# Kernel tuning notes

Measured on AMD Instinct MI355X. Metric: run time of the kernel, lower is better.

Reference implementation:

```python
import jax, jax.numpy as jnp
import numpy as np

N, E, F, U, H = 10000, 160000, 128, 128, 8
BN_EPS = 1e-3  # keras BatchNormalization default


def _batch_norm(x, gamma, beta):
    # GraphBatchNormalization in training mode: stats over the flat node/edge axis
    mean = jnp.mean(x, axis=0, keepdims=True)
    var = jnp.var(x, axis=0, keepdims=True)
    return (x - mean) * jax.lax.rsqrt(var + BN_EPS) * gamma + beta


def setup_inputs() -> dict:
    key = jax.random.key(0)
    k = jax.random.split(key, 12)
    s = 0.1  # weight init scale
    return {
        "node_attributes": jax.random.normal(k[0], (N, F), jnp.float32),
        "edge_attributes": jax.random.normal(k[1], (E, F), jnp.float32),
        "edge_indices": jax.random.randint(k[2], (E, 2), 0, N, jnp.int32),
        "W_edge": jax.random.normal(k[3], (3 * F, U), jnp.float32) * s,
        "b_edge": jnp.zeros((U,), jnp.float32),
        "gamma_e": jnp.ones((U,), jnp.float32),
        "beta_e": jnp.zeros((U,), jnp.float32),
        "W_node": jax.random.normal(k[4], (F, U), jnp.float32) * s,
        "b_node": jnp.zeros((U,), jnp.float32),
        "gamma_n": jnp.ones((U,), jnp.float32),
        "beta_n": jnp.zeros((U,), jnp.float32),
        "W_att": jax.random.normal(k[5], (H, F, U), jnp.float32) * s,
        "b_att": jnp.zeros((H, U), jnp.float32),
        "a_att": jax.random.normal(k[6], (H, 3 * U), jnp.float32) * s,
        "gru_kernel": jax.random.normal(k[7], (U, 3 * U), jnp.float32) * s,
        "gru_rkernel": jax.random.normal(k[8], (U, 3 * U), jnp.float32) * s,
        "gru_bias": jnp.zeros((2, 3 * U), jnp.float32),
    }


def reference(node_attributes, edge_attributes, edge_indices, W_edge, b_edge,
              gamma_e, beta_e, W_node, b_node, gamma_n, beta_n,
              W_att, b_att, a_att, gru_kernel, gru_rkernel, gru_bias):
    dst = edge_indices[:, 0]  # receiving (ingoing) node per edge
    src = edge_indices[:, 1]  # sending (outgoing) node per edge

    # gather -> concat -> edge MLP -> graph batch norm
    edge_in = node_attributes[src]   # GatherNodesOutgoing
    edge_out = node_attributes[dst]  # GatherNodesIngoing
    edge_concat = jnp.concatenate([edge_in, edge_out, edge_attributes], axis=-1)  # [E, 3F]
    edge_updated = jax.nn.relu(edge_concat @ W_edge + b_edge)
    edge_updated = _batch_norm(edge_updated, gamma_e, beta_e)  # [E, U]

    # multi-head GAT attention over edges, aggregated to receiving node
    z = jnp.einsum('nf,hfu->hnu', node_attributes, W_att) + b_att[:, None, :]  # [H,N,U]
    a_src, a_dst, a_edge = jnp.split(a_att, 3, axis=-1)  # each [H,U]
    s_src = jnp.einsum('hnu,hu->hn', z, a_src)[:, src]           # [H,E]
    s_dst = jnp.einsum('hnu,hu->hn', z, a_dst)[:, dst]           # [H,E]
    s_edge = jnp.einsum('eu,hu->he', edge_updated, a_edge)       # [H,E]
    logits = jax.nn.leaky_relu(s_src + s_dst + s_edge, 0.2)

    seg_max = jax.vmap(lambda l: jax.ops.segment_max(l, dst, num_segments=N))(logits)  # [H,N]
    ex = jnp.exp(logits - seg_max[:, dst])
    den = jax.vmap(lambda e: jax.ops.segment_sum(e, dst, num_segments=N))(ex)          # [H,N]
    alpha = ex / den[:, dst]                                                            # [H,E]

    msgs = alpha[:, :, None] * z[:, src]  # [H,E,U]
    agg = jax.vmap(lambda m: jax.ops.segment_sum(m, dst, num_segments=N))(msgs)  # [H,N,U]
    node_attended = jax.nn.relu(jnp.mean(agg, axis=0))  # [N,U]

    # node MLP + graph batch norm
    node_updated = jax.nn.relu(node_attributes @ W_node + b_node)
    node_updated = _batch_norm(node_updated, gamma_n, beta_n)  # [N,U]

    # GRU update (keras GRUCell, reset_after=True): input=node_attended, state=node_updated
    mx = node_attended @ gru_kernel + gru_bias[0]
    mi = node_updated @ gru_rkernel + gru_bias[1]
    xz, xr, xh = jnp.split(mx, 3, axis=-1)
    rz, rr, rh = jnp.split(mi, 3, axis=-1)
    zg = jax.nn.sigmoid(xz + rz)
    rg = jax.nn.sigmoid(xr + rr)
    hh = jnp.tanh(xh + rg * rh)
    node_final = zg * node_updated + (1.0 - zg) * hh

    return node_final, edge_updated
```

## Files before the change

kernel.cpp:

```cpp
#include <hip/hip_runtime.h>
#include <hip/hip_bf16.h>

#define NN 10000
#define EE 160000
#define FF 128
#define UU 128
#define HH 8
#define BN_EPS 1e-3f

typedef __attribute__((ext_vector_type(8))) short bf16x8;
typedef __attribute__((ext_vector_type(8))) unsigned short u16x8;
typedef __attribute__((ext_vector_type(4))) float f32x4;

static __device__ __forceinline__ unsigned short f2bf(float f) {
    unsigned u = __float_as_uint(f);
    u += 0x7fffu + ((u >> 16) & 1u);
    return (unsigned short)(u >> 16);
}
static __device__ __forceinline__ float bf2f(unsigned short b) {
    return __uint_as_float((unsigned)b << 16);
}

__global__ void k_prep(const float* __restrict__ node, unsigned short* __restrict__ node_bf,
                       const float* __restrict__ We, unsigned short* __restrict__ WtE,
                       const float* __restrict__ Wn, unsigned short* __restrict__ WnT,
                       const float* __restrict__ Watt, unsigned short* __restrict__ WtA,
                       const float* __restrict__ Wk, const float* __restrict__ Wr,
                       unsigned short* __restrict__ WcT) {
    int b = blockIdx.x, t = threadIdx.x;
    if (b < 1250) {
        int i = b * 256 + t;
        float4 v = reinterpret_cast<const float4*>(node)[i];
        ushort4 o;
        o.x = f2bf(v.x); o.y = f2bf(v.y); o.z = f2bf(v.z); o.w = f2bf(v.w);
        reinterpret_cast<ushort4*>(node_bf)[i] = o;
    } else if (b < 1442) {
        int i = (b - 1250) * 256 + t;
        int s = i >> 14, rem = i & 16383, u = rem >> 7, k = rem & 127;
        WtE[i] = f2bf(We[(s * 128 + k) * 128 + u]);
    } else if (b < 1506) {
        int i = (b - 1442) * 256 + t;
        int k = i >> 7, u = i & 127;
        WnT[u * 128 + k] = f2bf(Wn[i]);
    } else if (b < 2018) {
        int i = (b - 1506) * 256 + t;
        int h = i >> 14, rem = i & 16383, f = rem >> 7, u = rem & 127;
        WtA[h * 16384 + u * 128 + f] = f2bf(Watt[i]);
    } else {
        int i = (b - 2018) * 256 + t;
        int c = i >> 8, k = i & 255;
        float v;
        if (c < 256)       v = (k < 128) ? Wk[k * 384 + c] : Wr[(k - 128) * 384 + c];
        else if (c < 384)  v = (k < 128) ? Wk[k * 384 + c] : 0.f;
        else               v = (k < 128) ? 0.f : Wr[(k - 128) * 384 + (c - 128)];
        WcT[c * 256 + k] = f2bf(v);
    }
}

__global__ void k_hist(const int* __restrict__ eidx, int* __restrict__ cnt, int E) {
    int e = blockIdx.x * 256 + threadIdx.x;
    if (e < E) atomicAdd(&cnt[eidx[2 * e]], 1);
}

__global__ void k_scan(const int* __restrict__ cnt, int* __restrict__ off,
                       int* __restrict__ cursor, int N) {
    __shared__ int wpre[16];
    __shared__ int runsh;
    int t = threadIdx.x, lane = t & 63, wv = t >> 6;
    if (t == 0) { off[0] = 0; runsh = 0; }
    __syncthreads();
    for (int base = 0; base < N; base += 1024) {
        int x = (base + t < N) ? cnt[base + t] : 0;
        int s = x;
#pragma unroll
        for (int o = 1; o < 64; o <<= 1) {
            int v = __shfl_up(s, o, 64);
            if (lane >= o) s += v;
        }
        if (lane == 63) wpre[wv] = s;
        __syncthreads();
        if (t == 0) {
            int acc = runsh;
#pragma unroll
            for (int i = 0; i < 16; ++i) { int tmp = wpre[i]; wpre[i] = acc; acc += tmp; }
            runsh = acc;
        }
        __syncthreads();
        int inc = s + wpre[wv];
        if (base + t < N) {
            off[base + t + 1] = inc;
            cursor[base + t] = inc - x;
        }
        __syncthreads();
    }
}

__global__ void k_scatter(const int* __restrict__ eidx, int* __restrict__ cursor,
                          int* __restrict__ elist, int E) {
    int e = blockIdx.x * 256 + threadIdx.x;
    if (e < E) {
        int d = eidx[2 * e];
        int p = atomicAdd(&cursor[d], 1);
        elist[p] = e;
    }
}

__global__ void __launch_bounds__(256) k_z8(
        const unsigned short* __restrict__ node_bf, const unsigned short* __restrict__ WtA,
        const float* __restrict__ batt, const float* __restrict__ aatt,
        unsigned short* __restrict__ zt, float* __restrict__ s_src, float* __restrict__ s_dst) {
    __shared__ unsigned short lds[16 * 1032];
    int n0 = blockIdx.x * 16;
    int t = threadIdx.x;
    {
        int r = t >> 4, c = t & 15;
        *reinterpret_cast<uint4*>(&lds[r * 136 + c * 8]) =
            *reinterpret_cast<const uint4*>(node_bf + (size_t)(n0 + r) * 128 + c * 8);
    }
    __syncthreads();

    int wid = t >> 6, lane = t & 63;
    int lr = lane & 15, lg = lane >> 4;

    f32x4 acc[2][8];
#pragma unroll
    for (int hh = 0; hh < 2; ++hh)
#pragma unroll
        for (int nt = 0; nt < 8; ++nt) acc[hh][nt] = (f32x4){0.f, 0.f, 0.f, 0.f};

#pragma unroll
    for (int ks = 0; ks < 4; ++ks) {
        int kb = ks * 32 + lg * 8;
        bf16x8 a = *reinterpret_cast<const bf16x8*>(&lds[lr * 136 + kb]);
#pragma unroll
        for (int hh = 0; hh < 2; ++hh) {
            const unsigned short* Wh = WtA + (size_t)(wid * 2 + hh) * 16384;
#pragma unroll
            for (int nt = 0; nt < 8; ++nt) {
                bf16x8 b = *reinterpret_cast<const bf16x8*>(Wh + (size_t)(nt * 16 + lr) * 128 + kb);
                acc[hh][nt] = __builtin_amdgcn_mfma_f32_16x16x32_bf16(a, b, acc[hh][nt], 0, 0, 0);
            }
        }
    }

    __syncthreads();
    float ps[2][4], pd[2][4];
#pragma unroll
    for (int hh = 0; hh < 2; ++hh)
#pragma unroll
        for (int r = 0; r < 4; ++r) { ps[hh][r] = 0.f; pd[hh][r] = 0.f; }

#pragma unroll
    for (int hh = 0; hh < 2; ++hh) {
        int head = wid * 2 + hh;
#pragma unroll
        for (int nt = 0; nt < 8; ++nt) {
            int col = nt * 16 + lr;
            float bias = batt[head * 128 + col];
            float as = aatt[head * 384 + col];
            float ad = aatt[head * 384 + 128 + col];
#pragma unroll
            for (int r = 0; r < 4; ++r) {
                int row = lg * 4 + r;
                float zval = acc[hh][nt][r] + bias;
                lds[row * 1032 + ((col * 8) ^ ((row & 3) << 4)) + head] = f2bf(zval);
                ps[hh][r] = fmaf(zval, as, ps[hh][r]);
                pd[hh][r] = fmaf(zval, ad, pd[hh][r]);
            }
        }
    }
#pragma unroll
    for (int o = 1; o < 16; o <<= 1) {
#pragma unroll
        for (int hh = 0; hh < 2; ++hh)
#pragma unroll
            for (int r = 0; r < 4; ++r) {
                ps[hh][r] += __shfl_xor(ps[hh][r], o, 64);
                pd[hh][r] += __shfl_xor(pd[hh][r], o, 64);
            }
    }
    if (lr == 0) {
#pragma unroll
        for (int hh = 0; hh < 2; ++hh) {
            int head = wid * 2 + hh;
#pragma unroll
            for (int r = 0; r < 4; ++r) {
                int n = n0 + lg * 4 + r;
                s_src[n * 8 + head] = ps[hh][r];
                s_dst[n * 8 + head] = pd[hh][r];
            }
        }
    }
    __syncthreads();
    for (int q = t; q < 16 * 128; q += 256) {
        int row = q >> 7, c = q & 127;
        *reinterpret_cast<uint4*>(&zt[(size_t)(n0 + row) * 1024 + c * 8]) =
            *reinterpret_cast<const uint4*>(&lds[row * 1032 + ((c * 8) ^ ((row & 3) << 4))]);
    }
}

__global__ void __launch_bounds__(256) k_p12_mfma(
        const unsigned short* __restrict__ node_bf, const unsigned short* __restrict__ WtE,
        unsigned short* __restrict__ p12, int N) {
    __shared__ unsigned short ash[64][136];
    int n0 = blockIdx.x * 64;
    int s = blockIdx.y;
    int t = threadIdx.x;
    for (int q = t; q < 64 * 16; q += 256) {
        int r = q >> 4, c = q & 15;
        int n = n0 + r; if (n >= N) n = N - 1;
        *reinterpret_cast<uint4*>(&ash[r][c * 8]) =
            *reinterpret_cast<const uint4*>(node_bf + (size_t)n * 128 + c * 8);
    }
    __syncthreads();

    int wid = t >> 6, lane = t & 63;
    int wm = wid >> 1, wn = wid & 1;
    int lr = lane & 15, lg = lane >> 4;

    f32x4 acc[2][4];
#pragma unroll
    for (int m = 0; m < 2; ++m)
#pragma unroll
        for (int n = 0; n < 4; ++n) acc[m][n] = (f32x4){0.f, 0.f, 0.f, 0.f};

    const unsigned short* Wh = WtE + (size_t)s * 16384;
#pragma unroll
    for (int ks = 0; ks < 4; ++ks) {
        int kb = ks * 32 + lg * 8;
        bf16x8 a0 = *reinterpret_cast<const bf16x8*>(&ash[wm * 32 + lr][kb]);
        bf16x8 a1 = *reinterpret_cast<const bf16x8*>(&ash[wm * 32 + 16 + lr][kb]);
        bf16x8 b[4];
#pragma unroll
        for (int n = 0; n < 4; ++n)
            b[n] = *reinterpret_cast<const bf16x8*>(Wh + (size_t)(wn * 64 + n * 16 + lr) * 128 + kb);
#pragma unroll
        for (int n = 0; n < 4; ++n) {
            acc[0][n] = __builtin_amdgcn_mfma_f32_16x16x32_bf16(a0, b[n], acc[0][n], 0, 0, 0);
            acc[1][n] = __builtin_amdgcn_mfma_f32_16x16x32_bf16(a1, b[n], acc[1][n], 0, 0, 0);
        }
    }

    __syncthreads();
    unsigned short* ot = &ash[0][0];
#pragma unroll
    for (int n = 0; n < 4; ++n) {
        int col = wn * 64 + n * 16 + lr;
#pragma unroll
        for (int m = 0; m < 2; ++m) {
            int rowb = wm * 32 + m * 16 + lg * 4;
#pragma unroll
            for (int r = 0; r < 4; ++r)
                ot[(rowb + r) * 136 + col] = f2bf(acc[m][n][r]);
        }
    }
    __syncthreads();
    for (int q = t; q < 64 * 16; q += 256) {
        int r = q >> 4, c = q & 15;
        int row = n0 + r;
        if (row < N)
            *reinterpret_cast<uint4*>(&p12[(size_t)row * 256 + s * 128 + c * 8]) =
                *reinterpret_cast<const uint4*>(&ot[r * 136 + c * 8]);
    }
}

__global__ void __launch_bounds__(256) k_pe_comb(
        const float* __restrict__ eattr, const unsigned short* __restrict__ WtE,
        const float* __restrict__ be, const unsigned short* __restrict__ p12,
        const int* __restrict__ eidx, unsigned short* __restrict__ ebuf,
        float* __restrict__ part) {
    __shared__ unsigned short ash[64][136];
    __shared__ int sd[128];
    __shared__ float sbuf[4][64], qbuf[4][64];
    int e0 = blockIdx.x * 64;
    int t = threadIdx.x;
    if (t < 128) sd[t] = eidx[e0 * 2 + t];
    for (int q = t; q < 64 * 32; q += 256) {
        int r = q >> 5, c = q & 31;
        float4 v = *reinterpret_cast<const float4*>(eattr + (size_t)(e0 + r) * 128 + c * 4);
        ushort4 o;
        o.x = f2bf(v.x); o.y = f2bf(v.y); o.z = f2bf(v.z); o.w = f2bf(v.w);
        *reinterpret_cast<ushort4*>(&ash[r][c * 4]) = o;
    }
    __syncthreads();

    int wid = t >> 6, lane = t & 63;
    int wm = wid >> 1, wn = wid & 1;
    int lr = lane & 15, lg = lane >> 4;

    f32x4 acc[2][4];
#pragma unroll
    for (int m = 0; m < 2; ++m)
#pragma unroll
        for (int n = 0; n < 4; ++n) acc[m][n] = (f32x4){0.f, 0.f, 0.f, 0.f};

    const unsigned short* Wh = WtE + (size_t)2 * 16384;
#pragma unroll
    for (int ks = 0; ks < 4; ++ks) {
        int kb = ks * 32 + lg * 8;
        bf16x8 a0 = *reinterpret_cast<const bf16x8*>(&ash[wm * 32 + lr][kb]);
        bf16x8 a1 = *reinterpret_cast<const bf16x8*>(&ash[wm * 32 + 16 + lr][kb]);
        bf16x8 b[4];
#pragma unroll
        for (int n = 0; n < 4; ++n)
            b[n] = *reinterpret_cast<const bf16x8*>(Wh + (size_t)(wn * 64 + n * 16 + lr) * 128 + kb);
#pragma unroll
        for (int n = 0; n < 4; ++n) {
            acc[0][n] = __builtin_amdgcn_mfma_f32_16x16x32_bf16(a0, b[n], acc[0][n], 0, 0, 0);
            acc[1][n] = __builtin_amdgcn_mfma_f32_16x16x32_bf16(a1, b[n], acc[1][n], 0, 0, 0);
        }
    }

    __syncthreads();
    for (int q = t; q < 64 * 16; q += 256) {
        int r = q >> 4, c = q & 15;
        int dst = sd[r * 2], src = sd[r * 2 + 1];
        u16x8 a = *reinterpret_cast<const u16x8*>(p12 + (size_t)src * 256 + c * 8);
        u16x8 b = *reinterpret_cast<const u16x8*>(p12 + (size_t)dst * 256 + 128 + c * 8);
        u16x8 o;
#pragma unroll
        for (int j = 0; j < 8; ++j) o[j] = f2bf(bf2f(a[j]) + bf2f(b[j]));
        *reinterpret_cast<u16x8*>(&ash[r][c * 8]) = o;
    }
    __syncthreads();

    unsigned short* ot = &ash[0][0];
    float s[4] = {0.f, 0.f, 0.f, 0.f}, q[4] = {0.f, 0.f, 0.f, 0.f};
#pragma unroll
    for (int n = 0; n < 4; ++n) {
        int col = wn * 64 + n * 16 + lr;
        float bias = be[col];
#pragma unroll
        for (int m = 0; m < 2; ++m) {
            int rowb = wm * 32 + m * 16 + lg * 4;
#pragma unroll
            for (int r = 0; r < 4; ++r) {
                int row = rowb + r;
                float v = acc[m][n][r] + bias + bf2f(ot[row * 136 + col]);
                v = v > 0.f ? v : 0.f;
                ot[row * 136 + col] = f2bf(v);
                s[n] += v;
                q[n] += v * v;
            }
        }
    }
#pragma unroll
    for (int n = 0; n < 4; ++n) {
        s[n] += __shfl_xor(s[n], 16, 64);
        s[n] += __shfl_xor(s[n], 32, 64);
        q[n] += __shfl_xor(q[n], 16, 64);
        q[n] += __shfl_xor(q[n], 32, 64);
    }
    if (lane < 16) {
#pragma unroll
        for (int n = 0; n < 4; ++n) {
            sbuf[wid][n * 16 + lane] = s[n];
            qbuf[wid][n * 16 + lane] = q[n];
        }
    }
    __syncthreads();
    for (int q2 = t; q2 < 64 * 16; q2 += 256) {
        int r = q2 >> 4, c = q2 & 15;
        *reinterpret_cast<uint4*>(&ebuf[(size_t)(e0 + r) * 128 + c * 8]) =
            *reinterpret_cast<const uint4*>(&ot[r * 136 + c * 8]);
    }
    if (t < 128) {
        int half = t >> 6, c = t & 63;
        part[(size_t)blockIdx.x * 256 + t] = sbuf[half][c] + sbuf[2 + half][c];
        part[(size_t)blockIdx.x * 256 + 128 + t] = qbuf[half][c] + qbuf[2 + half][c];
    }
}

__global__ void __launch_bounds__(256) k_node_mlp_mfma(
        const unsigned short* __restrict__ node_bf, const unsigned short* __restrict__ WnT,
        const float* __restrict__ bn, unsigned short* __restrict__ nupd_bf,
        float* __restrict__ part, int N) {
    __shared__ unsigned short ash[64][136];
    __shared__ float sbuf[4][64], qbuf[4][64];
    int n0 = blockIdx.x * 64;
    int t = threadIdx.x;
    for (int q = t; q < 64 * 16; q += 256) {
        int r = q >> 4, c = q & 15;
        int n = n0 + r; if (n >= N) n = N - 1;
        *reinterpret_cast<uint4*>(&ash[r][c * 8]) =
            *reinterpret_cast<const uint4*>(node_bf + (size_t)n * 128 + c * 8);
    }
    __syncthreads();

    int wid = t >> 6, lane = t & 63;
    int wm = wid >> 1, wn = wid & 1;
    int lr = lane & 15, lg = lane >> 4;

    f32x4 acc[2][4];
#pragma unroll
    for (int m = 0; m < 2; ++m)
#pragma unroll
        for (int n = 0; n < 4; ++n) acc[m][n] = (f32x4){0.f, 0.f, 0.f, 0.f};

#pragma unroll
    for (int ks = 0; ks < 4; ++ks) {
        int kb = ks * 32 + lg * 8;
        bf16x8 a0 = *reinterpret_cast<const bf16x8*>(&ash[wm * 32 + lr][kb]);
        bf16x8 a1 = *reinterpret_cast<const bf16x8*>(&ash[wm * 32 + 16 + lr][kb]);
        bf16x8 b[4];
#pragma unroll
        for (int n = 0; n < 4; ++n)
            b[n] = *reinterpret_cast<const bf16x8*>(WnT + (size_t)(wn * 64 + n * 16 + lr) * 128 + kb);
#pragma unroll
        for (int n = 0; n < 4; ++n) {
            acc[0][n] = __builtin_amdgcn_mfma_f32_16x16x32_bf16(a0, b[n], acc[0][n], 0, 0, 0);
            acc[1][n] = __builtin_amdgcn_mfma_f32_16x16x32_bf16(a1, b[n], acc[1][n], 0, 0, 0);
        }
    }

    __syncthreads();
    unsigned short* ot = &ash[0][0];
    float s[4] = {0.f, 0.f, 0.f, 0.f}, q[4] = {0.f, 0.f, 0.f, 0.f};
#pragma unroll
    for (int n = 0; n < 4; ++n) {
        int col = wn * 64 + n * 16 + lr;
        float bias = bn[col];
#pragma unroll
        for (int m = 0; m < 2; ++m) {
            int rowb = wm * 32 + m * 16 + lg * 4;
#pragma unroll
            for (int r = 0; r < 4; ++r) {
                int row = n0 + rowb + r;
                float v = acc[m][n][r] + bias;
                v = v > 0.f ? v : 0.f;
                ot[(rowb + r) * 136 + col] = f2bf(v);
                if (row < N) { s[n] += v; q[n] += v * v; }
            }
        }
    }
#pragma unroll
    for (int n = 0; n < 4; ++n) {
        s[n] += __shfl_xor(s[n], 16, 64);
        s[n] += __shfl_xor(s[n], 32, 64);
        q[n] += __shfl_xor(q[n], 16, 64);
        q[n] += __shfl_xor(q[n], 32, 64);
    }
    if (lane < 16) {
#pragma unroll
        for (int n = 0; n < 4; ++n) {
            sbuf[wid][n * 16 + lane] = s[n];
            qbuf[wid][n * 16 + lane] = q[n];
        }
    }
    __syncthreads();
    for (int q2 = t; q2 < 64 * 16; q2 += 256) {
        int r = q2 >> 4, c = q2 & 15;
        int row = n0 + r;
        if (row < N)
            *reinterpret_cast<uint4*>(&nupd_bf[(size_t)row * 128 + c * 8]) =
                *reinterpret_cast<const uint4*>(&ot[r * 136 + c * 8]);
    }
    if (t < 128) {
        int half = t >> 6, c = t & 63;
        part[(size_t)blockIdx.x * 256 + t] = sbuf[half][c] + sbuf[2 + half][c];
        part[(size_t)blockIdx.x * 256 + 128 + t] = qbuf[half][c] + qbuf[2 + half][c];
    }
}

__global__ void k_bn_fin(const float* __restrict__ part, int nblk, float invcnt,
                         const float* __restrict__ g, const float* __restrict__ b,
                         float* __restrict__ scale, float* __restrict__ shift) {
    int u = blockIdx.x;
    int t = threadIdx.x;
    float s = 0.f, q = 0.f;
    for (int i = t; i < nblk; i += 256) {
        s += part[(size_t)i * 256 + u];
        q += part[(size_t)i * 256 + 128 + u];
    }
    __shared__ float ls[4], lq[4];
    for (int o = 32; o > 0; o >>= 1) {
        s += __shfl_down(s, o, 64);
        q += __shfl_down(q, o, 64);
    }
    int lane = t & 63, w = t >> 6;
    if (lane == 0) { ls[w] = s; lq[w] = q; }
    __syncthreads();
    if (t == 0) {
        float S = ls[0] + ls[1] + ls[2] + ls[3];
        float Q = lq[0] + lq[1] + lq[2] + lq[3];
        float mean = S * invcnt;
        float var = Q * invcnt - mean * mean;
        float inv = rsqrtf(var + BN_EPS);
        float sc = g[u] * inv;
        scale[u] = sc;
        shift[u] = b[u] - mean * sc;
    }
}

__global__ void __launch_bounds__(256) k_edge_final(
        const unsigned short* __restrict__ ebuf, const float* __restrict__ scale,
        const float* __restrict__ shift, const float* __restrict__ aatt,
        float* __restrict__ eout, float* __restrict__ s_edge) {
    int t = threadIdx.x;
    int w = t >> 6, lane = t & 63;
    int q = lane & 31, half = lane >> 5;
    int e = blockIdx.x * 8 + w * 2 + half;

    float4 sc = *reinterpret_cast<const float4*>(scale + q * 4);
    float4 sh = *reinterpret_cast<const float4*>(shift + q * 4);
    float4 a4[8];
#pragma unroll
    for (int h = 0; h < 8; ++h)
        a4[h] = *reinterpret_cast<const float4*>(aatt + h * 384 + 256 + q * 4);

    ushort4 xb = *reinterpret_cast<const ushort4*>(ebuf + (size_t)e * 128 + q * 4);
    float4 x;
    x.x = bf2f(xb.x) * sc.x + sh.x;
    x.y = bf2f(xb.y) * sc.y + sh.y;
    x.z = bf2f(xb.z) * sc.z + sh.z;
    x.w = bf2f(xb.w) * sc.w + sh.w;
    *reinterpret_cast<float4*>(eout + (size_t)e * 128 + q * 4) = x;

    float v[8];
#pragma unroll
    for (int h = 0; h < 8; ++h)
        v[h] = x.x * a4[h].x + x.y * a4[h].y + x.z * a4[h].z + x.w * a4[h].w;
#pragma unroll
    for (int o = 1; o < 32; o <<= 1) {
#pragma unroll
        for (int h = 0; h < 8; ++h) v[h] += __shfl_xor(v[h], o, 64);
    }
    if (q == 0) {
#pragma unroll
        for (int h = 0; h < 8; ++h) s_edge[e * 8 + h] = v[h];
    }
}

__global__ void k_agg(const unsigned short* __restrict__ zt, const float* __restrict__ s_src,
                      const float* __restrict__ s_dst, const float* __restrict__ s_edge,
                      const int* __restrict__ off, const int* __restrict__ elist,
                      const int* __restrict__ eidx, unsigned short* __restrict__ cat) {
    int n = blockIdx.x;
    int t = threadIdx.x;
    int beg = off[n], end = off[n + 1];
    int deg = end - beg;
    if (deg == 0) { cat[(size_t)n * 256 + t] = 0; return; }

    float sdh[8];
#pragma unroll
    for (int h = 0; h < 8; ++h) sdh[h] = s_dst[n * 8 + h];

    __shared__ float lred[16];
    __shared__ float wbuf[128][8];
    __shared__ int snbuf[128];

    float mx[8], den[8];
#pragma unroll
    for (int h = 0; h < 8; ++h) { mx[h] = -1e30f; den[h] = 0.f; }

    int lane = t & 63, w = t >> 6;

    for (int c0 = 0; c0 < deg; c0 += 128) {
        int cn = min(128, deg - c0);
        bool act = t < cn;
        int e = 0, sn = 0;
        if (act) { e = elist[beg + c0 + t]; sn = eidx[2 * e + 1]; }
        float lg[8];
#pragma unroll
        for (int h = 0; h < 8; ++h) {
            float x = act ? (s_src[sn * 8 + h] + sdh[h] + s_edge[e * 8 + h]) : -1e30f;
            lg[h] = x >= 0.f ? x : 0.2f * x;
        }
        float cm[8];
#pragma unroll
        for (int h = 0; h < 8; ++h) cm[h] = lg[h];
        for (int o = 32; o > 0; o >>= 1) {
#pragma unroll
            for (int h = 0; h < 8; ++h) cm[h] = fmaxf(cm[h], __shfl_down(cm[h], o, 64));
        }
        if (lane == 0) {
#pragma unroll
            for (int h = 0; h < 8; ++h) lred[w * 8 + h] = cm[h];
        }
        __syncthreads();
#pragma unroll
        for (int h = 0; h < 8; ++h) cm[h] = fmaxf(lred[h], lred[8 + h]);
        __syncthreads();
        float cs[8];
#pragma unroll
        for (int h = 0; h < 8; ++h) cs[h] = act ? __expf(lg[h] - cm[h]) : 0.f;
        for (int o = 32; o > 0; o >>= 1) {
#pragma unroll
            for (int h = 0; h < 8; ++h) cs[h] += __shfl_down(cs[h], o, 64);
        }
        if (lane == 0) {
#pragma unroll
            for (int h = 0; h < 8; ++h) lred[w * 8 + h] = cs[h];
        }
        __syncthreads();
#pragma unroll
        for (int h = 0; h < 8; ++h) {
            float csum = lred[h] + lred[8 + h];
            float nm = fmaxf(mx[h], cm[h]);
            den[h] = den[h] * __expf(mx[h] - nm) + csum * __expf(cm[h] - nm);
            mx[h] = nm;
        }
        __syncthreads();
    }
    float inv[8];
#pragma unroll
    for (int h = 0; h < 8; ++h) inv[h] = 1.f / den[h];

    float acc = 0.f;
    for (int c0 = 0; c0 < deg; c0 += 128) {
        int cn = min(128, deg - c0);
        if (t < cn) {
            int e = elist[beg + c0 + t];
            int sn = eidx[2 * e + 1];
            snbuf[t] = sn;
#pragma unroll
            for (int h = 0; h < 8; ++h) {
                float x = s_src[sn * 8 + h] + sdh[h] + s_edge[e * 8 + h];
                x = x >= 0.f ? x : 0.2f * x;
                wbuf[t][h] = __expf(x - mx[h]) * inv[h];
            }
        }
        __syncthreads();
        for (int i = 0; i < cn; ++i) {
            int sn = snbuf[i];
            u16x8 zv = *reinterpret_cast<const u16x8*>(zt + (size_t)sn * 1024 + t * 8);
            float4 w0 = *reinterpret_cast<const float4*>(&wbuf[i][0]);
            float4 w1 = *reinterpret_cast<const float4*>(&wbuf[i][4]);
            acc = fmaf(w0.x, bf2f(zv[0]), acc);
            acc = fmaf(w0.y, bf2f(zv[1]), acc);
            acc = fmaf(w0.z, bf2f(zv[2]), acc);
            acc = fmaf(w0.w, bf2f(zv[3]), acc);
            acc = fmaf(w1.x, bf2f(zv[4]), acc);
            acc = fmaf(w1.y, bf2f(zv[5]), acc);
            acc = fmaf(w1.z, bf2f(zv[6]), acc);
            acc = fmaf(w1.w, bf2f(zv[7]), acc);
        }
        __syncthreads();
    }
    cat[(size_t)n * 256 + t] = f2bf(fmaxf(acc * 0.125f, 0.f));
}

__global__ void k_gru_pre(const unsigned short* __restrict__ nupd_bf, const float* __restrict__ scale,
                          const float* __restrict__ shift, unsigned short* __restrict__ cat,
                          float* __restrict__ ush) {
    int i = blockIdx.x * 256 + threadIdx.x;
    if (i >= NN * 32) return;
    int n = i >> 5, j4 = (i & 31) * 4;
    ushort4 ub_in = *reinterpret_cast<const ushort4*>(nupd_bf + (size_t)n * 128 + j4);
    float4 sc = *reinterpret_cast<const float4*>(scale + j4);
    float4 sh = *reinterpret_cast<const float4*>(shift + j4);
    float4 uv;
    uv.x = bf2f(ub_in.x) * sc.x + sh.x;
    uv.y = bf2f(ub_in.y) * sc.y + sh.y;
    uv.z = bf2f(ub_in.z) * sc.z + sh.z;
    uv.w = bf2f(ub_in.w) * sc.w + sh.w;
    ushort4 ub;
    ub.x = f2bf(uv.x); ub.y = f2bf(uv.y); ub.z = f2bf(uv.z); ub.w = f2bf(uv.w);
    *reinterpret_cast<ushort4*>(cat + (size_t)n * 256 + 128 + j4) = ub;
    *reinterpret_cast<float4*>(ush + (size_t)n * 128 + j4) = uv;
}

__global__ void __launch_bounds__(256) k_gru_mm(
        const unsigned short* __restrict__ cat, const unsigned short* __restrict__ WcT,
        float* __restrict__ S, int N) {
    __shared__ unsigned short ash[64][264];
    int n0 = blockIdx.x * 64;
    int g = blockIdx.y;
    int t = threadIdx.x;
    for (int q = t; q < 64 * 32; q += 256) {
        int r = q >> 5, c = q & 31;
        int n = n0 + r; if (n >= N) n = N - 1;
        *reinterpret_cast<uint4*>(&ash[r][c * 8]) =
            *reinterpret_cast<const uint4*>(cat + (size_t)n * 256 + c * 8);
    }
    __syncthreads();

    int wid = t >> 6, lane = t & 63;
    int wm = wid >> 1, wn = wid & 1;
    int lr = lane & 15, lg = lane >> 4;

    f32x4 acc[2][4];
#pragma unroll
    for (int m = 0; m < 2; ++m)
#pragma unroll
        for (int n = 0; n < 4; ++n) acc[m][n] = (f32x4){0.f, 0.f, 0.f, 0.f};

    const unsigned short* Wg = WcT + (size_t)g * 128 * 256;
#pragma unroll
    for (int ks = 0; ks < 8; ++ks) {
        int kb = ks * 32 + lg * 8;
        bf16x8 a0 = *reinterpret_cast<const bf16x8*>(&ash[wm * 32 + lr][kb]);
        bf16x8 a1 = *reinterpret_cast<const bf16x8*>(&ash[wm * 32 + 16 + lr][kb]);
        bf16x8 b[4];
#pragma unroll
        for (int n = 0; n < 4; ++n)
            b[n] = *reinterpret_cast<const bf16x8*>(Wg + (size_t)(wn * 64 + n * 16 + lr) * 256 + kb);
#pragma unroll
        for (int n = 0; n < 4; ++n) {
            acc[0][n] = __builtin_amdgcn_mfma_f32_16x16x32_bf16(a0, b[n], acc[0][n], 0, 0, 0);
            acc[1][n] = __builtin_amdgcn_mfma_f32_16x16x32_bf16(a1, b[n], acc[1][n], 0, 0, 0);
        }
    }

    __syncthreads();
    float* otf = reinterpret_cast<float*>(&ash[0][0]);
#pragma unroll
    for (int n = 0; n < 4; ++n) {
        int col = wn * 64 + n * 16 + lr;
#pragma unroll
        for (int m = 0; m < 2; ++m) {
            int rowb = wm * 32 + m * 16 + lg * 4;
#pragma unroll
            for (int r = 0; r < 4; ++r)
                otf[(rowb + r) * 132 + col] = acc[m][n][r];
        }
    }
    __syncthreads();
    for (int q = t; q < 64 * 32; q += 256) {
        int r = q >> 5, c = q & 31;
        int row = n0 + r;
        if (row < N)
            *reinterpret_cast<float4*>(&S[(size_t)row * 512 + g * 128 + c * 4]) =
                *reinterpret_cast<const float4*>(&otf[r * 132 + c * 4]);
    }
}

__global__ void __launch_bounds__(256) k_gru_gates(
        const float* __restrict__ S, const float* __restrict__ ush,
        const float* __restrict__ gbias, float* __restrict__ outp) {
    int t = threadIdx.x;
    int n = blockIdx.x * 2 + (t >> 7);
    int u = t & 127;
    const float* b0 = gbias;
    const float* b1 = gbias + 384;
    float s0 = S[(size_t)n * 512 + u];
    float s1 = S[(size_t)n * 512 + 128 + u];
    float xh = S[(size_t)n * 512 + 256 + u];
    float rh = S[(size_t)n * 512 + 384 + u];
    float zg = 1.f / (1.f + __expf(-(s0 + b0[u] + b1[u])));
    float rg = 1.f / (1.f + __expf(-(s1 + b0[128 + u] + b1[128 + u])));
    float hh = tanhf(xh + b0[256 + u] + rg * (rh + b1[256 + u]));
    float uv = ush[(size_t)n * 128 + u];
    outp[(size_t)n * 128 + u] = zg * uv + (1.f - zg) * hh;
}

extern "C" void kernel_launch(void* const* d_in, const int* in_sizes, int n_in,
                              void* d_out, int out_size, void* d_ws, size_t ws_size,
                              hipStream_t stream) {
    const float* node    = (const float*)d_in[0];
    const float* eattr   = (const float*)d_in[1];
    const int*   eidx    = (const int*)d_in[2];
    const float* We      = (const float*)d_in[3];
    const float* be      = (const float*)d_in[4];
    const float* gamma_e = (const float*)d_in[5];
    const float* beta_e  = (const float*)d_in[6];
    const float* Wn      = (const float*)d_in[7];
    const float* bnb     = (const float*)d_in[8];
    const float* gamma_n = (const float*)d_in[9];
    const float* beta_n  = (const float*)d_in[10];
    const float* Watt    = (const float*)d_in[11];
    const float* batt    = (const float*)d_in[12];
    const float* aatt    = (const float*)d_in[13];
    const float* Wk      = (const float*)d_in[14];
    const float* Wr      = (const float*)d_in[15];
    const float* gbias   = (const float*)d_in[16];

    float* out_node = (float*)d_out;
    float* out_edge = out_node + (size_t)NN * UU;

    char* wp = (char*)d_ws;
    auto alloc = [&](size_t bytes) {
        void* p = (void*)wp;
        wp += (bytes + 255) / 256 * 256;
        return p;
    };
    unsigned short* zt   = (unsigned short*)alloc((size_t)NN * 1024 * 2);
    unsigned short* ebuf = (unsigned short*)alloc((size_t)EE * 128 * 2);
    float* s_src   = (float*)alloc((size_t)NN * 8 * 4);
    float* s_dst   = (float*)alloc((size_t)NN * 8 * 4);
    float* s_edge  = (float*)alloc((size_t)EE * 8 * 4);
    float* part_e  = (float*)alloc((size_t)2500 * 256 * 4);
    float* part_n  = (float*)alloc((size_t)157 * 256 * 4);
    float* scale_e = (float*)alloc(512);
    float* shift_e = (float*)alloc(512);
    float* scale_n = (float*)alloc(512);
    float* shift_n = (float*)alloc(512);
    unsigned short* nupd_bf = (unsigned short*)alloc((size_t)NN * 128 * 2);
    float* ush     = (float*)alloc((size_t)NN * 128 * 4);
    float* Sbuf    = (float*)alloc((size_t)NN * 512 * 4);
    int*   cnt     = (int*)alloc((size_t)NN * 4);
    int*   offs    = (int*)alloc((size_t)(NN + 1) * 4);
    int*   cursor  = (int*)alloc((size_t)NN * 4);
    int*   elist   = (int*)alloc((size_t)EE * 4);
    unsigned short* node_bf = (unsigned short*)alloc((size_t)NN * 128 * 2);
    unsigned short* WtE     = (unsigned short*)alloc((size_t)3 * 128 * 128 * 2);
    unsigned short* WtA     = (unsigned short*)alloc((size_t)8 * 128 * 128 * 2);
    unsigned short* WnT     = (unsigned short*)alloc((size_t)128 * 128 * 2);
    unsigned short* WcT     = (unsigned short*)alloc((size_t)512 * 256 * 2);
    unsigned short* cat     = (unsigned short*)alloc((size_t)NN * 256 * 2);
    unsigned short* p12     = (unsigned short*)alloc((size_t)NN * 256 * 2);

    hipMemsetAsync(cnt, 0, (size_t)NN * 4, stream);
    k_hist<<<(EE + 255) / 256, 256, 0, stream>>>(eidx, cnt, EE);
    k_scan<<<1, 1024, 0, stream>>>(cnt, offs, cursor, NN);
    k_scatter<<<(EE + 255) / 256, 256, 0, stream>>>(eidx, cursor, elist, EE);

    k_prep<<<2530, 256, 0, stream>>>(node, node_bf, We, WtE, Wn, WnT, Watt, WtA, Wk, Wr, WcT);

    k_p12_mfma<<<dim3((NN + 63) / 64, 2), 256, 0, stream>>>(node_bf, WtE, p12, NN);
    k_pe_comb<<<EE / 64, 256, 0, stream>>>(eattr, WtE, be, p12, eidx, ebuf, part_e);
    k_bn_fin<<<128, 256, 0, stream>>>(part_e, EE / 64, 1.f / (float)EE,
                                      gamma_e, beta_e, scale_e, shift_e);
    k_edge_final<<<EE / 8, 256, 0, stream>>>(ebuf, scale_e, shift_e, aatt, out_edge, s_edge);

    k_z8<<<NN / 16, 256, 0, stream>>>(node_bf, WtA, batt, aatt, zt, s_src, s_dst);
    k_agg<<<NN, 128, 0, stream>>>(zt, s_src, s_dst, s_edge, offs, elist, eidx, cat);

    k_node_mlp_mfma<<<(NN + 63) / 64, 256, 0, stream>>>(node_bf, WnT, bnb, nupd_bf, part_n, NN);
    k_bn_fin<<<128, 256, 0, stream>>>(part_n, (NN + 63) / 64, 1.f / (float)NN,
                                      gamma_n, beta_n, scale_n, shift_n);

    k_gru_pre<<<(NN * 32 + 255) / 256, 256, 0, stream>>>(nupd_bf, scale_n, shift_n, cat, ush);
    k_gru_mm<<<dim3((NN + 63) / 64, 4), 256, 0, stream>>>(cat, WcT, Sbuf, NN);
    k_gru_gates<<<NN / 2, 256, 0, stream>>>(Sbuf, ush, gbias, out_node);
}
```

Before: 279.7 us.

## Fuse softmax and aggregation into one online pass; reorder edge-combine before MFMA

The per-node attention aggregation now uses an online softmax: each chunk's exp weights are computed once against the running max, stored to shared memory, and used right away to accumulate per-head sums that are rescaled when the max changes. This removes the second pass over the edge list, which recomputed the logits with gathers of s_src and s_edge. Normalization by the denominator moves to the end. In the edge kernel, the gathered p12 combination is written to a separate shared buffer before the MFMA, so the gather loads can overlap the eattr conversion. This costs extra LDS and per-head accumulator registers.

```diff
diff --git a/kernel.cpp b/kernel.cpp
--- a/kernel.cpp
+++ b/kernel.cpp
@@ -270,11 +270,13 @@
         const int* __restrict__ eidx, unsigned short* __restrict__ ebuf,
         float* __restrict__ part) {
     __shared__ unsigned short ash[64][136];
+    __shared__ unsigned short pcomb[64][136];
     __shared__ int sd[128];
     __shared__ float sbuf[4][64], qbuf[4][64];
     int e0 = blockIdx.x * 64;
     int t = threadIdx.x;
     if (t < 128) sd[t] = eidx[e0 * 2 + t];
+    __syncthreads();
     for (int q = t; q < 64 * 32; q += 256) {
         int r = q >> 5, c = q & 31;
         float4 v = *reinterpret_cast<const float4*>(eattr + (size_t)(e0 + r) * 128 + c * 4);
@@ -282,36 +284,6 @@
         o.x = f2bf(v.x); o.y = f2bf(v.y); o.z = f2bf(v.z); o.w = f2bf(v.w);
         *reinterpret_cast<ushort4*>(&ash[r][c * 4]) = o;
     }
-    __syncthreads();
-
-    int wid = t >> 6, lane = t & 63;
-    int wm = wid >> 1, wn = wid & 1;
-    int lr = lane & 15, lg = lane >> 4;
-
-    f32x4 acc[2][4];
-#pragma unroll
-    for (int m = 0; m < 2; ++m)
-#pragma unroll
-        for (int n = 0; n < 4; ++n) acc[m][n] = (f32x4){0.f, 0.f, 0.f, 0.f};
-
-    const unsigned short* Wh = WtE + (size_t)2 * 16384;
-#pragma unroll
-    for (int ks = 0; ks < 4; ++ks) {
-        int kb = ks * 32 + lg * 8;
-        bf16x8 a0 = *reinterpret_cast<const bf16x8*>(&ash[wm * 32 + lr][kb]);
-        bf16x8 a1 = *reinterpret_cast<const bf16x8*>(&ash[wm * 32 + 16 + lr][kb]);
-        bf16x8 b[4];
-#pragma unroll
-        for (int n = 0; n < 4; ++n)
-            b[n] = *reinterpret_cast<const bf16x8*>(Wh + (size_t)(wn * 64 + n * 16 + lr) * 128 + kb);
-#pragma unroll
-        for (int n = 0; n < 4; ++n) {
-            acc[0][n] = __builtin_amdgcn_mfma_f32_16x16x32_bf16(a0, b[n], acc[0][n], 0, 0, 0);
-            acc[1][n] = __builtin_amdgcn_mfma_f32_16x16x32_bf16(a1, b[n], acc[1][n], 0, 0, 0);
-        }
-    }
-
-    __syncthreads();
     for (int q = t; q < 64 * 16; q += 256) {
         int r = q >> 4, c = q & 15;
         int dst = sd[r * 2], src = sd[r * 2 + 1];
@@ -320,10 +292,38 @@
         u16x8 o;
 #pragma unroll
         for (int j = 0; j < 8; ++j) o[j] = f2bf(bf2f(a[j]) + bf2f(b[j]));
-        *reinterpret_cast<u16x8*>(&ash[r][c * 8]) = o;
-    }
-    __syncthreads();
-
+        *reinterpret_cast<u16x8*>(&pcomb[r][c * 8]) = o;
+    }
+    __syncthreads();
+
+    int wid = t >> 6, lane = t & 63;
+    int wm = wid >> 1, wn = wid & 1;
+    int lr = lane & 15, lg = lane >> 4;
+
+    f32x4 acc[2][4];
+#pragma unroll
+    for (int m = 0; m < 2; ++m)
+#pragma unroll
+        for (int n = 0; n < 4; ++n) acc[m][n] = (f32x4){0.f, 0.f, 0.f, 0.f};
+
+    const unsigned short* Wh = WtE + (size_t)2 * 16384;
+#pragma unroll
+    for (int ks = 0; ks < 4; ++ks) {
+        int kb = ks * 32 + lg * 8;
+        bf16x8 a0 = *reinterpret_cast<const bf16x8*>(&ash[wm * 32 + lr][kb]);
+        bf16x8 a1 = *reinterpret_cast<const bf16x8*>(&ash[wm * 32 + 16 + lr][kb]);
+        bf16x8 b[4];
+#pragma unroll
+        for (int n = 0; n < 4; ++n)
+            b[n] = *reinterpret_cast<const bf16x8*>(Wh + (size_t)(wn * 64 + n * 16 + lr) * 128 + kb);
+#pragma unroll
+        for (int n = 0; n < 4; ++n) {
+            acc[0][n] = __builtin_amdgcn_mfma_f32_16x16x32_bf16(a0, b[n], acc[0][n], 0, 0, 0);
+            acc[1][n] = __builtin_amdgcn_mfma_f32_16x16x32_bf16(a1, b[n], acc[1][n], 0, 0, 0);
+        }
+    }
+
+    __syncthreads();
     unsigned short* ot = &ash[0][0];
     float s[4] = {0.f, 0.f, 0.f, 0.f}, q[4] = {0.f, 0.f, 0.f, 0.f};
 #pragma unroll
@@ -336,7 +336,7 @@
 #pragma unroll
             for (int r = 0; r < 4; ++r) {
                 int row = rowb + r;
-                float v = acc[m][n][r] + bias + bf2f(ot[row * 136 + col]);
+                float v = acc[m][n][r] + bias + bf2f(pcomb[row][col]);
                 v = v > 0.f ? v : 0.f;
                 ot[row * 136 + col] = f2bf(v);
                 s[n] += v;
@@ -549,9 +549,9 @@
     __shared__ float wbuf[128][8];
     __shared__ int snbuf[128];
 
-    float mx[8], den[8];
-#pragma unroll
-    for (int h = 0; h < 8; ++h) { mx[h] = -1e30f; den[h] = 0.f; }
+    float mx[8], den[8], accv[8];
+#pragma unroll
+    for (int h = 0; h < 8; ++h) { mx[h] = -1e30f; den[h] = 0.f; accv[h] = 0.f; }
 
     int lane = t & 63, w = t >> 6;
 
@@ -559,7 +559,7 @@
         int cn = min(128, deg - c0);
         bool act = t < cn;
         int e = 0, sn = 0;
-        if (act) { e = elist[beg + c0 + t]; sn = eidx[2 * e + 1]; }
+        if (act) { e = elist[beg + c0 + t]; sn = eidx[2 * e + 1]; snbuf[t] = sn; }
         float lg[8];
 #pragma unroll
         for (int h = 0; h < 8; ++h) {
@@ -581,9 +581,19 @@
 #pragma unroll
         for (int h = 0; h < 8; ++h) cm[h] = fmaxf(lred[h], lred[8 + h]);
         __syncthreads();
+        float nm[8], cw[8];
+#pragma unroll
+        for (int h = 0; h < 8; ++h) {
+            nm[h] = fmaxf(mx[h], cm[h]);
+            cw[h] = act ? __expf(lg[h] - nm[h]) : 0.f;
+        }
+        if (act) {
+#pragma unroll
+            for (int h = 0; h < 8; ++h) wbuf[t][h] = cw[h];
+        }
         float cs[8];
 #pragma unroll
-        for (int h = 0; h < 8; ++h) cs[h] = act ? __expf(lg[h] - cm[h]) : 0.f;
+        for (int h = 0; h < 8; ++h) cs[h] = cw[h];
         for (int o = 32; o > 0; o >>= 1) {
 #pragma unroll
             for (int h = 0; h < 8; ++h) cs[h] += __shfl_down(cs[h], o, 64);
@@ -595,49 +605,31 @@
         __syncthreads();
 #pragma unroll
         for (int h = 0; h < 8; ++h) {
-            float csum = lred[h] + lred[8 + h];
-            float nm = fmaxf(mx[h], cm[h]);
-            den[h] = den[h] * __expf(mx[h] - nm) + csum * __expf(cm[h] - nm);
-            mx[h] = nm;
-        }
-        __syncthreads();
-    }
-    float inv[8];
-#pragma unroll
-    for (int h = 0; h < 8; ++h) inv[h] = 1.f / den[h];
-
-    float acc = 0.f;
-    for (int c0 = 0; c0 < deg; c0 += 128) {
-        int cn = min(128, deg - c0);
-        if (t < cn) {
-            int e = elist[beg + c0 + t];
-            int sn = eidx[2 * e + 1];
-            snbuf[t] = sn;
-#pragma unroll
-            for (int h = 0; h < 8; ++h) {
-                float x = s_src[sn * 8 + h] + sdh[h] + s_edge[e * 8 + h];
-                x = x >= 0.f ? x : 0.2f * x;
-                wbuf[t][h] = __expf(x - mx[h]) * inv[h];
-            }
-        }
-        __syncthreads();
+            float so = __expf(mx[h] - nm[h]);
+            den[h] = den[h] * so + (lred[h] + lred[8 + h]);
+            accv[h] *= so;
+            mx[h] = nm[h];
+        }
         for (int i = 0; i < cn; ++i) {
-            int sn = snbuf[i];
-            u16x8 zv = *reinterpret_cast<const u16x8*>(zt + (size_t)sn * 1024 + t * 8);
+            int sn_i = snbuf[i];
+            u16x8 zv = *reinterpret_cast<const u16x8*>(zt + (size_t)sn_i * 1024 + t * 8);
             float4 w0 = *reinterpret_cast<const float4*>(&wbuf[i][0]);
             float4 w1 = *reinterpret_cast<const float4*>(&wbuf[i][4]);
-            acc = fmaf(w0.x, bf2f(zv[0]), acc);
-            acc = fmaf(w0.y, bf2f(zv[1]), acc);
-            acc = fmaf(w0.z, bf2f(zv[2]), acc);
-            acc = fmaf(w0.w, bf2f(zv[3]), acc);
-            acc = fmaf(w1.x, bf2f(zv[4]), acc);
-            acc = fmaf(w1.y, bf2f(zv[5]), acc);
-            acc = fmaf(w1.z, bf2f(zv[6]), acc);
-            acc = fmaf(w1.w, bf2f(zv[7]), acc);
+            accv[0] = fmaf(w0.x, bf2f(zv[0]), accv[0]);
+            accv[1] = fmaf(w0.y, bf2f(zv[1]), accv[1]);
+            accv[2] = fmaf(w0.z, bf2f(zv[2]), accv[2]);
+            accv[3] = fmaf(w0.w, bf2f(zv[3]), accv[3]);
+            accv[4] = fmaf(w1.x, bf2f(zv[4]), accv[4]);
+            accv[5] = fmaf(w1.y, bf2f(zv[5]), accv[5]);
+            accv[6] = fmaf(w1.z, bf2f(zv[6]), accv[6]);
+            accv[7] = fmaf(w1.w, bf2f(zv[7]), accv[7]);
         }
         __syncthreads();
     }
-    cat[(size_t)n * 256 + t] = f2bf(fmaxf(acc * 0.125f, 0.f));
+    float r = 0.f;
+#pragma unroll
+    for (int h = 0; h < 8; ++h) r = fmaf(accv[h], 1.f / den[h], r);
+    cat[(size_t)n * 256 + t] = f2bf(fmaxf(r * 0.125f, 0.f));
 }
 
 __global__ void k_gru_pre(const unsigned short* __restrict__ nupd_bf, const float* __restrict__ scale,
```

Measured after the change: 280.6 us. About the same (+0.3%).
